# Performance work log

Measured on AMD Instinct MI355X. Metric: run time of the kernel, lower is better.

Reference implementation:

```python
import jax, jax.numpy as jnp
import numpy as np

N_SVC, N_NODE, N_POD = 50000, 20000, 100000
F = 128          # svc/instance/node feature dims (all 128 per init_kwargs)
HID = 128        # hidden_size
OUT = 64         # out_channel
E_SVC, E_PN, E_NP = 1600000, 100000, 100000


def _graph_conv(x, src, dst, n_src, n_dst, W, b):
    """DGL GraphConv with norm='both': D_dst^{-1/2} A D_src^{-1/2} X W + b."""
    ones = jnp.ones(src.shape[0], dtype=x.dtype)
    deg_src = jnp.clip(jax.ops.segment_sum(ones, src, num_segments=n_src), 1.0)
    deg_dst = jnp.clip(jax.ops.segment_sum(ones, dst, num_segments=n_dst), 1.0)
    # normalize at source, gather, scatter-sum to dst, normalize at dst
    h = x * jax.lax.rsqrt(deg_src)[:, None]          # [n_src, F]
    msg = h[src]                                      # [E, F] gather (memory-bound)
    agg = jax.ops.segment_sum(msg, dst, num_segments=n_dst)  # [n_dst, F]
    agg = agg * jax.lax.rsqrt(deg_dst)[:, None]
    return agg @ W + b                                # [n_dst, HID]


def _leaky(h):
    return jnp.where(h > 0, h, 0.01 * h)


def setup_inputs() -> dict:
    key = jax.random.key(0)
    ks = jax.random.split(key, 16)
    d = {
        "x_svc": jax.random.normal(ks[0], (N_SVC, F), jnp.float32),
        "x_pod": jax.random.normal(ks[1], (N_POD, F), jnp.float32),
        "x_node": jax.random.normal(ks[2], (N_NODE, F), jnp.float32),
        "svc_src": jax.random.randint(ks[3], (E_SVC,), 0, N_SVC, jnp.int32),
        "svc_dst": jax.random.randint(ks[4], (E_SVC,), 0, N_SVC, jnp.int32),
        "pod_node_src": jax.random.randint(ks[5], (E_PN,), 0, N_POD, jnp.int32),
        "pod_node_dst": jax.random.randint(ks[6], (E_PN,), 0, N_NODE, jnp.int32),
        "node_pod_src": jax.random.randint(ks[7], (E_NP,), 0, N_NODE, jnp.int32),
        "node_pod_dst": jax.random.randint(ks[8], (E_NP,), 0, N_POD, jnp.int32),
        # GraphConv weights per edge type
        "W_call": jax.random.normal(ks[9], (F, HID), jnp.float32) * (1.0 / np.sqrt(F)),
        "b_call": jnp.zeros((HID,), jnp.float32),
        "W_in": jax.random.normal(ks[10], (F, HID), jnp.float32) * (1.0 / np.sqrt(F)),
        "b_in": jnp.zeros((HID,), jnp.float32),
        "W_ni": jax.random.normal(ks[11], (F, HID), jnp.float32) * (1.0 / np.sqrt(F)),
        "b_ni": jnp.zeros((HID,), jnp.float32),
        # per-node-type output Linear (hidden -> out_channel)
        "W_lin_svc": jax.random.normal(ks[12], (HID, OUT), jnp.float32) * (1.0 / np.sqrt(HID)),
        "b_lin_svc": jnp.zeros((OUT,), jnp.float32),
        "W_lin_node": jax.random.normal(ks[13], (HID, OUT), jnp.float32) * (1.0 / np.sqrt(HID)),
        "b_lin_node": jnp.zeros((OUT,), jnp.float32),
        "W_lin_pod": jax.random.normal(ks[14], (HID, OUT), jnp.float32) * (1.0 / np.sqrt(HID)),
        "b_lin_pod": jnp.zeros((OUT,), jnp.float32),
    }
    return d


def reference(x_svc, x_pod, x_node,
              svc_src, svc_dst, pod_node_src, pod_node_dst,
              node_pod_src, node_pod_dst,
              W_call, b_call, W_in, b_in, W_ni, b_ni,
              W_lin_svc, b_lin_svc, W_lin_node, b_lin_node,
              W_lin_pod, b_lin_pod):
    # HeteroGraphConv (sum aggregate; each dst type receives one edge type here)
    h_svc = _graph_conv(x_svc, svc_src, svc_dst, N_SVC, N_SVC, W_call, b_call)
    h_node = _graph_conv(x_pod, pod_node_src, pod_node_dst, N_POD, N_NODE, W_in, b_in)
    h_pod = _graph_conv(x_node, node_pod_src, node_pod_dst, N_NODE, N_POD, W_ni, b_ni)
    # per-node-type LeakyReLU + Linear
    o_svc = _leaky(h_svc) @ W_lin_svc + b_lin_svc    # [N_SVC, OUT]
    o_node = _leaky(h_node) @ W_lin_node + b_lin_node  # [N_NODE, OUT]
    o_pod = _leaky(h_pod) @ W_lin_pod + b_lin_pod    # [N_POD, OUT]
    return jnp.concatenate([o_svc, o_node, o_pod], axis=0)  # [N_SVC+N_NODE+N_POD, OUT]
```

## Files before the change

kernel.cpp:

```cpp
#include <hip/hip_runtime.h>

typedef __attribute__((ext_vector_type(8))) short short8;
typedef __attribute__((ext_vector_type(4))) float floatx4;

#define N_SVC  50000
#define N_NODE 20000
#define N_POD  100000
#define E_SVC  1600000
#define E_PN   100000
#define E_NP   100000
#define N_TOT  170000
#define E_TOT  1800000
#define NBUCK  1329
#define NBLK   256
#define PER_BLK 7032
#define P_SVC_BASE  0
#define P_NODE_BASE 50048
#define P_POD_BASE  70080
#define P_TOT       170112
#define SVC_WAVES   50048
#define SVC_HALF    25024
#define SVC_HBLK    6256
#define NP_WAVES    30016
#define NP_BLOCKS   7504

__device__ __forceinline__ unsigned short f2bf(float f) {
  union { float f; unsigned u; } v; v.f = f;
  unsigned r = v.u + 0x7FFFu + ((v.u >> 16) & 1u);
  return (unsigned short)(r >> 16);
}
__device__ __forceinline__ unsigned pack_bf2(float a, float b) {
  return (unsigned)f2bf(a) | ((unsigned)f2bf(b) << 16);
}
__device__ __forceinline__ float bfl(unsigned u) { union { unsigned u; float f; } v; v.u = u << 16; return v.f; }
__device__ __forceinline__ float bfh(unsigned u) { union { unsigned u; float f; } v; v.u = u & 0xFFFF0000u; return v.f; }

__device__ __forceinline__ int dbase_of(int b) {
  if (b <= 391) return b * 6144;
  if (b <= 547) return 2402304 + (b - 391) * 1536;
  return 2641920 + (b - 547) * 512;
}
#define DST_CAP_TOT 3042304
__device__ __forceinline__ int sbase_of(int b) {
  if (b <= 391) return b * 6144;
  if (b <= 1171) return 2402304 + (b - 391) * 512;
  return 2801664 + (b - 1171) * 1536;
}
#define SRC_CAP_TOT 3044352

__device__ __forceinline__ void load_edge(int i,
    const int* __restrict__ svcS, const int* __restrict__ svcD,
    const int* __restrict__ pnS, const int* __restrict__ pnD,
    const int* __restrict__ npS, const int* __restrict__ npD,
    int& S, int& D) {
  if (i < E_SVC)             { S = svcS[i];                         D = svcD[i]; }
  else if (i < E_SVC + E_PN) { int j = i - E_SVC;        S = pnS[j] + 50000;  D = pnD[j] + 50000; }
  else                       { int j = i - E_SVC - E_PN; S = npS[j] + 150000; D = npD[j] + 70000; }
}

__global__ void wprep_init(const float* __restrict__ W0, const float* __restrict__ W1,
                           const float* __restrict__ W2, const float* __restrict__ L0,
                           const float* __restrict__ L1, const float* __restrict__ L2,
                           unsigned short* __restrict__ Wt, unsigned short* __restrict__ Wt2,
                           int* __restrict__ dcur, int* __restrict__ scur) {
  int i = blockIdx.x * 256 + threadIdx.x;
  if (i < NBUCK) { dcur[i] = dbase_of(i); scur[i] = sbase_of(i); }
  if (i < 3 * 16384) {
    int t = i / 16384, r = i % 16384, n = r / 128, k = r % 128;
    const float* W = (t == 0) ? W0 : ((t == 1) ? W1 : W2);
    Wt[i] = f2bf(W[k * 128 + n]);
  } else if (i < 3 * 16384 + 3 * 8192) {
    int j = i - 3 * 16384;
    int t = j / 8192, r = j % 8192, n = r / 128, k = r % 128;
    const float* L = (t == 0) ? L0 : ((t == 1) ? L1 : L2);
    Wt2[j] = f2bf(L[k * 64 + n]);
  }
}

__global__ __launch_bounds__(1024) void scatter_onepass(
    const int* __restrict__ svcS, const int* __restrict__ svcD,
    const int* __restrict__ pnS, const int* __restrict__ pnD,
    const int* __restrict__ npS, const int* __restrict__ npD,
    int* __restrict__ dcur, int* __restrict__ scur,
    unsigned* __restrict__ dstbuf, unsigned char* __restrict__ srcbuf) {
  __shared__ int ldc[NBUCK], lsc[NBUCK];
  const int tid = threadIdx.x;
  for (int t = tid; t < NBUCK; t += 1024) { ldc[t] = 0; lsc[t] = 0; }
  __syncthreads();
  const int lo = blockIdx.x * PER_BLK;
  const int hi = (lo + PER_BLK < E_TOT) ? lo + PER_BLK : E_TOT;
  int Sv[7], Dv[7];
  #pragma unroll
  for (int k = 0; k < 7; ++k) {
    int e = lo + tid + k * 1024;
    if (e < hi) {
      load_edge(e, svcS, svcD, pnS, pnD, npS, npD, Sv[k], Dv[k]);
      atomicAdd(&ldc[Dv[k] >> 7], 1);
      atomicAdd(&lsc[Sv[k] >> 7], 1);
    } else Sv[k] = -1;
  }
  __syncthreads();
  for (int t = tid; t < NBUCK; t += 1024) {
    int c = ldc[t];  ldc[t] = c ? atomicAdd(&dcur[t], c) : 0;
    int c2 = lsc[t]; lsc[t] = c2 ? atomicAdd(&scur[t], c2) : 0;
  }
  __syncthreads();
  #pragma unroll
  for (int k = 0; k < 7; ++k) {
    if (Sv[k] >= 0) {
      int p = atomicAdd(&ldc[Dv[k] >> 7], 1);
      dstbuf[p] = ((unsigned)(Dv[k] & 127) << 18) | (unsigned)Sv[k];
      int q = atomicAdd(&lsc[Sv[k] >> 7], 1);
      srcbuf[q] = (unsigned char)(Sv[k] & 127);
    }
  }
}

__global__ __launch_bounds__(256) void finalize_all(
    const int* __restrict__ dcur, const int* __restrict__ scur,
    const unsigned* __restrict__ dstbuf, const unsigned char* __restrict__ srcbuf,
    int2* __restrict__ rowrange, int* __restrict__ csr, int* __restrict__ cnt_src) {
  __shared__ int lcnt[128], lcur[128];
  __shared__ int s_w0;
  const int tid = threadIdx.x;
  if (blockIdx.x < NBUCK) {
    const int b = blockIdx.x;
    const int base = dbase_of(b);
    const int cnt = dcur[b] - base;
    if (tid < 128) lcnt[tid] = 0;
    __syncthreads();
    for (int e = tid; e < cnt; e += 256) atomicAdd(&lcnt[dstbuf[base + e] >> 18], 1);
    __syncthreads();
    int excl = 0, v = 0;
    if (tid < 128) {
      v = lcnt[tid];
      int lane = tid & 63;
      int x = v;
      #pragma unroll
      for (int off = 1; off < 64; off <<= 1) {
        int y = __shfl_up(x, off, 64);
        if (lane >= off) x += y;
      }
      excl = x - v;
      if (tid == 63) s_w0 = x;
    }
    __syncthreads();
    if (tid < 128) {
      if (tid >= 64) excl += s_w0;
      lcur[tid] = excl;
      int u = b * 128 + tid;
      if (u < N_TOT) rowrange[u] = make_int2(base + excl, base + excl + v);
    }
    __syncthreads();
    for (int e = tid; e < cnt; e += 256) {
      unsigned wv = dstbuf[base + e];
      int p = atomicAdd(&lcur[wv >> 18], 1);
      csr[base + p] = (int)(wv & 0x3FFFFu);
    }
  } else {
    const int b = blockIdx.x - NBUCK;
    const int base = sbase_of(b);
    const int cnt = scur[b] - base;
    if (tid < 128) lcnt[tid] = 0;
    __syncthreads();
    for (int e = tid; e < cnt; e += 256) atomicAdd(&lcnt[srcbuf[base + e]], 1);
    __syncthreads();
    if (tid < 128) {
      int u = b * 128 + tid;
      if (u < N_TOT) cnt_src[u] = lcnt[tid];
    }
  }
}

__global__ void normalize_cast(const float* __restrict__ xs, const int* __restrict__ cs,
                               unsigned* __restrict__ Xn) {
  int i = blockIdx.x * blockDim.x + threadIdx.x;
  if (i >= N_SVC * 32) return;
  int row = i >> 5, c4 = i & 31;
  const float* src = xs + (size_t)row * 128;
  int cc = cs[row]; if (cc < 1) cc = 1;
  float r = rsqrtf((float)cc);
  float4 v = ((const float4*)src)[c4];
  uint2 o;
  o.x = pack_bf2(v.x * r, v.y * r);
  o.y = pack_bf2(v.z * r, v.w * r);
  *(uint2*)(Xn + (size_t)row * 64 + c4 * 2) = o;
}

#define ACC8(v) { a0 += bfl(v.x); a1 += bfh(v.x); a2 += bfl(v.y); a3 += bfh(v.y); \
                  a4 += bfl(v.z); a5 += bfh(v.z); a6 += bfl(v.w); a7 += bfh(v.w); }

__global__ __launch_bounds__(256) void aggregate_svc(
    const unsigned* __restrict__ Xn, const int2* __restrict__ rowrange,
    const int* __restrict__ csr, unsigned* __restrict__ aggb, int rbase) {
  const int lane = threadIdx.x & 63;
  const int gw = rbase + blockIdx.x * 4 + (threadIdx.x >> 6);
  const int grp = lane >> 4, l16 = lane & 15;
  const unsigned* Xb = Xn + l16 * 4;
  unsigned* orow = aggb + (size_t)gw * 64 + l16 * 4;
  if (gw >= 50000) {
    if (gw < SVC_WAVES && grp == 0) *(uint4*)orow = (uint4){0u, 0u, 0u, 0u};
    return;
  }
  int2 rr = rowrange[gw];
  int beg = rr.x, end = rr.y;
  int deg = end - beg;
  float a0 = 0.f, a1 = 0.f, a2 = 0.f, a3 = 0.f, a4 = 0.f, a5 = 0.f, a6 = 0.f, a7 = 0.f;
  int e = beg;
  for (; e + 16 <= end; e += 16) {
    int s0 = csr[e + grp];
    int s1 = csr[e + 4 + grp];
    int s2 = csr[e + 8 + grp];
    int s3 = csr[e + 12 + grp];
    uint4 v0 = *(const uint4*)(Xb + (unsigned)s0 * 64);
    uint4 v1 = *(const uint4*)(Xb + (unsigned)s1 * 64);
    uint4 v2 = *(const uint4*)(Xb + (unsigned)s2 * 64);
    uint4 v3 = *(const uint4*)(Xb + (unsigned)s3 * 64);
    ACC8(v0) ACC8(v1) ACC8(v2) ACC8(v3)
  }
  for (; e + 8 <= end; e += 8) {
    int s0 = csr[e + grp];
    int s1 = csr[e + 4 + grp];
    uint4 v0 = *(const uint4*)(Xb + (unsigned)s0 * 64);
    uint4 v1 = *(const uint4*)(Xb + (unsigned)s1 * 64);
    ACC8(v0) ACC8(v1)
  }
  for (; e + 4 <= end; e += 4) {
    int s = csr[e + grp];
    uint4 v = *(const uint4*)(Xb + (unsigned)s * 64);
    ACC8(v)
  }
  if (grp < end - e) {
    int s = csr[e + grp];
    uint4 v = *(const uint4*)(Xb + (unsigned)s * 64);
    ACC8(v)
  }
  a0 += __shfl_xor(a0, 32, 64); a1 += __shfl_xor(a1, 32, 64);
  a2 += __shfl_xor(a2, 32, 64); a3 += __shfl_xor(a3, 32, 64);
  a4 += __shfl_xor(a4, 32, 64); a5 += __shfl_xor(a5, 32, 64);
  a6 += __shfl_xor(a6, 32, 64); a7 += __shfl_xor(a7, 32, 64);
  a0 += __shfl_xor(a0, 16, 64); a1 += __shfl_xor(a1, 16, 64);
  a2 += __shfl_xor(a2, 16, 64); a3 += __shfl_xor(a3, 16, 64);
  a4 += __shfl_xor(a4, 16, 64); a5 += __shfl_xor(a5, 16, 64);
  a6 += __shfl_xor(a6, 16, 64); a7 += __shfl_xor(a7, 16, 64);
  float rd = rsqrtf((float)(deg < 1 ? 1 : deg));
  if (grp == 0) {
    uint4 o;
    o.x = pack_bf2(a0 * rd, a1 * rd);
    o.y = pack_bf2(a2 * rd, a3 * rd);
    o.z = pack_bf2(a4 * rd, a5 * rd);
    o.w = pack_bf2(a6 * rd, a7 * rd);
    *(uint4*)orow = o;
  }
}

__global__ __launch_bounds__(256) void aggregate_np(
    const float* __restrict__ xp, const float* __restrict__ xn,
    const int* __restrict__ cnt_src, const int2* __restrict__ rowrange,
    const int* __restrict__ csr, unsigned* __restrict__ aggb) {
  const int lane = threadIdx.x & 63;
  const int w = blockIdx.x * 4 + (threadIdx.x >> 6);
  const int grp = lane >> 4, l16 = lane & 15;
  const int row = SVC_WAVES + w * 4 + grp;
  if (row >= P_TOT) return;
  int u; bool valid; const float* Xf; int soff;
  if (row < P_POD_BASE) { u = row - 48; valid = (row - P_NODE_BASE) < 20000; Xf = xp; soff = 50000; }
  else                  { u = row - 80; valid = (row - P_POD_BASE) < 100000; Xf = xn; soff = 150000; }
  unsigned* orow = aggb + (size_t)row * 64 + l16 * 4;
  if (!valid) {
    *(uint4*)orow = (uint4){0u, 0u, 0u, 0u};
    return;
  }
  const float* Xb = Xf + l16 * 8;
  int2 rr = rowrange[u];
  int beg = rr.x, end = rr.y;
  int deg = end - beg;
  float a0 = 0.f, a1 = 0.f, a2 = 0.f, a3 = 0.f, a4 = 0.f, a5 = 0.f, a6 = 0.f, a7 = 0.f;
  int e = beg;
  for (; e + 2 <= end; e += 2) {
    int s0 = csr[e], s1 = csr[e + 1];
    int c0 = cnt_src[s0]; if (c0 < 1) c0 = 1;
    int c1 = cnt_src[s1]; if (c1 < 1) c1 = 1;
    float r0 = rsqrtf((float)c0), r1 = rsqrtf((float)c1);
    const float* p0 = Xb + (size_t)(s0 - soff) * 128;
    const float* p1 = Xb + (size_t)(s1 - soff) * 128;
    float4 u0 = *(const float4*)p0;
    float4 u1 = *(const float4*)(p0 + 4);
    float4 w0 = *(const float4*)p1;
    float4 w1 = *(const float4*)(p1 + 4);
    a0 += u0.x * r0 + w0.x * r1; a1 += u0.y * r0 + w0.y * r1;
    a2 += u0.z * r0 + w0.z * r1; a3 += u0.w * r0 + w0.w * r1;
    a4 += u1.x * r0 + w1.x * r1; a5 += u1.y * r0 + w1.y * r1;
    a6 += u1.z * r0 + w1.z * r1; a7 += u1.w * r0 + w1.w * r1;
  }
  if (e < end) {
    int s = csr[e];
    int c = cnt_src[s]; if (c < 1) c = 1;
    float r = rsqrtf((float)c);
    const float* p = Xb + (size_t)(s - soff) * 128;
    float4 u0 = *(const float4*)p;
    float4 u1 = *(const float4*)(p + 4);
    a0 += u0.x * r; a1 += u0.y * r; a2 += u0.z * r; a3 += u0.w * r;
    a4 += u1.x * r; a5 += u1.y * r; a6 += u1.z * r; a7 += u1.w * r;
  }
  float rd = rsqrtf((float)(deg < 1 ? 1 : deg));
  uint4 o;
  o.x = pack_bf2(a0 * rd, a1 * rd);
  o.y = pack_bf2(a2 * rd, a3 * rd);
  o.z = pack_bf2(a4 * rd, a5 * rd);
  o.w = pack_bf2(a6 * rd, a7 * rd);
  *(uint4*)orow = o;
}

__global__ __launch_bounds__(256) void gemm_fused(
    const unsigned short* __restrict__ aggb,
    const unsigned short* __restrict__ Wt,
    const unsigned short* __restrict__ Wt2,
    const float* __restrict__ b0, const float* __restrict__ b1, const float* __restrict__ b2,
    const float* __restrict__ l0, const float* __restrict__ l1, const float* __restrict__ l2,
    float* __restrict__ out) {
  __shared__ __align__(16) unsigned short sW1[128 * 136];
  __shared__ __align__(16) unsigned short sH[4][16 * 136];
  const int bid = blockIdx.x;
  int t, bl, nb, ntile, padbase, outbase, mcnt;
  if (bid < 226)      { t = 0; bl = bid;       nb = 226; ntile = 782;  padbase = P_SVC_BASE;  outbase = 0;     mcnt = 50000; }
  else if (bid < 316) { t = 1; bl = bid - 226; nb = 90;  ntile = 313;  padbase = P_NODE_BASE; outbase = 50000; mcnt = 20000; }
  else                { t = 2; bl = bid - 316; nb = 452; ntile = 1563; padbase = P_POD_BASE;  outbase = 70000; mcnt = 100000; }
  const float* bp = (t == 0) ? b0 : ((t == 1) ? b1 : b2);
  const float* lp = (t == 0) ? l0 : ((t == 1) ? l1 : l2);

  const unsigned short* W1g = Wt + t * 16384;
  for (int uu = threadIdx.x; uu < 2048; uu += 256) {
    short8 v = *(const short8*)(W1g + uu * 8);
    *(short8*)(&sW1[(uu >> 4) * 136 + (uu & 15) * 8]) = v;
  }
  const int wv = threadIdx.x >> 6, lane = threadIdx.x & 63;
  const int quad = lane >> 4, l16 = lane & 15;

  const unsigned short* W2g = Wt2 + t * 8192;
  short8 w2f[4][4];
  #pragma unroll
  for (int n = 0; n < 4; n++)
    #pragma unroll
    for (int kt = 0; kt < 4; kt++)
      w2f[n][kt] = *(const short8*)(W2g + (n * 16 + l16) * 128 + kt * 32 + quad * 8);
  float bias1[8], bias2[4];
  #pragma unroll
  for (int n = 0; n < 8; n++) bias1[n] = bp[n * 16 + l16];
  #pragma unroll
  for (int n = 0; n < 4; n++) bias2[n] = lp[n * 16 + l16];
  __syncthreads();

  const unsigned short* Abase = aggb + (size_t)padbase * 128
                              + (size_t)(wv * 16 + l16) * 128 + quad * 8;
  short8 afc[4];
  if (bl < ntile) {
    const unsigned short* Ar = Abase + (size_t)bl * 8192;
    #pragma unroll
    for (int kt = 0; kt < 4; kt++) afc[kt] = *(const short8*)(Ar + kt * 32);
  }
  for (int tile = bl; tile < ntile; tile += nb) {
    short8 afn[4] = {afc[0], afc[1], afc[2], afc[3]};
    int tn = tile + nb;
    if (tn < ntile) {
      const unsigned short* Ar = Abase + (size_t)tn * 8192;
      #pragma unroll
      for (int kt = 0; kt < 4; kt++) afn[kt] = *(const short8*)(Ar + kt * 32);
    }
    floatx4 acc[8];
    #pragma unroll
    for (int n = 0; n < 8; n++) acc[n] = (floatx4){0.f, 0.f, 0.f, 0.f};
    #pragma unroll
    for (int kt = 0; kt < 4; kt++) {
      #pragma unroll
      for (int n = 0; n < 8; n++) {
        short8 bf = *(const short8*)(&sW1[(n * 16 + l16) * 136 + kt * 32 + quad * 8]);
        acc[n] = __builtin_amdgcn_mfma_f32_16x16x32_bf16(afc[kt], bf, acc[n], 0, 0, 0);
      }
    }
    #pragma unroll
    for (int n = 0; n < 8; n++) {
      #pragma unroll
      for (int i = 0; i < 4; i++) {
        float h = acc[n][i] + bias1[n];
        h = (h > 0.f) ? h : 0.01f * h;
        sH[wv][(quad * 4 + i) * 136 + n * 16 + l16] = f2bf(h);
      }
    }
    floatx4 acc2[4];
    #pragma unroll
    for (int n = 0; n < 4; n++) acc2[n] = (floatx4){0.f, 0.f, 0.f, 0.f};
    #pragma unroll
    for (int kt = 0; kt < 4; kt++) {
      short8 af = *(const short8*)(&sH[wv][l16 * 136 + kt * 32 + quad * 8]);
      #pragma unroll
      for (int n = 0; n < 4; n++)
        acc2[n] = __builtin_amdgcn_mfma_f32_16x16x32_bf16(af, w2f[n][kt], acc2[n], 0, 0, 0);
    }
    int r0 = tile * 64 + wv * 16 + quad * 4;
    #pragma unroll
    for (int n = 0; n < 4; n++) {
      #pragma unroll
      for (int i = 0; i < 4; i++) {
        int r = r0 + i;
        if (r < mcnt) out[(size_t)(outbase + r) * 64 + n * 16 + l16] = acc2[n][i] + bias2[n];
      }
    }
    #pragma unroll
    for (int kt = 0; kt < 4; kt++) afc[kt] = afn[kt];
  }
}

extern "C" void kernel_launch(void* const* d_in, const int* in_sizes, int n_in,
                              void* d_out, int out_size, void* d_ws, size_t ws_size,
                              hipStream_t stream) {
  const float* x_svc  = (const float*)d_in[0];
  const float* x_pod  = (const float*)d_in[1];
  const float* x_node = (const float*)d_in[2];
  const int* svc_src  = (const int*)d_in[3];
  const int* svc_dst  = (const int*)d_in[4];
  const int* pn_src   = (const int*)d_in[5];
  const int* pn_dst   = (const int*)d_in[6];
  const int* np_src   = (const int*)d_in[7];
  const int* np_dst   = (const int*)d_in[8];
  const float* W_call = (const float*)d_in[9];
  const float* b_call = (const float*)d_in[10];
  const float* W_in   = (const float*)d_in[11];
  const float* b_in   = (const float*)d_in[12];
  const float* W_ni   = (const float*)d_in[13];
  const float* b_ni   = (const float*)d_in[14];
  const float* W_ls   = (const float*)d_in[15];
  const float* b_ls   = (const float*)d_in[16];
  const float* W_ln   = (const float*)d_in[17];
  const float* b_ln   = (const float*)d_in[18];
  const float* W_lp   = (const float*)d_in[19];
  const float* b_lp   = (const float*)d_in[20];
  float* out = (float*)d_out;

  char* ws = (char*)d_ws;
  int*  dcur     = (int*)(ws + 0);
  int*  scur     = (int*)(ws + 5504);
  int2* rowrange = (int2*)(ws + 11008);
  int*  cnt_src  = (int*)(ws + 1371008);
  int*  csr      = (int*)(ws + 2051072);
  unsigned short* Wt  = (unsigned short*)(ws + 14220288);
  unsigned short* Wt2 = (unsigned short*)(ws + 14318592);
  unsigned* Xn     = (unsigned*)(ws + 14367744);
  unsigned* dstbuf = (unsigned*)(ws + 14367744);
  unsigned char* srcbuf = (unsigned char*)(ws + 27180032);
  unsigned* aggb   = (unsigned*)(ws + 30224384);

  wprep_init<<<288, 256, 0, stream>>>(W_call, W_in, W_ni, W_ls, W_ln, W_lp,
                                      Wt, Wt2, dcur, scur);
  scatter_onepass<<<NBLK, 1024, 0, stream>>>(svc_src, svc_dst, pn_src, pn_dst,
                                             np_src, np_dst, dcur, scur, dstbuf, srcbuf);
  finalize_all<<<2 * NBUCK, 256, 0, stream>>>(dcur, scur, dstbuf, srcbuf,
                                              rowrange, csr, cnt_src);
  normalize_cast<<<6250, 256, 0, stream>>>(x_svc, cnt_src, Xn);
  aggregate_svc<<<SVC_HBLK, 256, 0, stream>>>(Xn, rowrange, csr, aggb, 0);
  aggregate_svc<<<SVC_HBLK, 256, 0, stream>>>(Xn, rowrange, csr, aggb, SVC_HALF);
  aggregate_np<<<NP_BLOCKS, 256, 0, stream>>>(x_pod, x_node, cnt_src, rowrange, csr, aggb);
  gemm_fused<<<768, 256, 0, stream>>>((const unsigned short*)aggb, Wt, Wt2,
                                      b_call, b_in, b_ni, b_ls, b_ln, b_lp, out);
}
```

Measured before the change: 307.0 us.

## Fuse normalize-cast into finalize and merge aggregation kernels into one launch

Folds the source-degree normalization and bf16 cast of svc features into the source-count blocks of finalize_all. Xn moves to its own workspace region so it no longer aliases dstbuf. The two svc aggregation launches and the pod/node aggregation launch become a single aggregate_all kernel that branches on wave index. The A-fragment register prefetch in gemm_fused is also removed. The goal is fewer kernel launches and inter-kernel gaps, at the cost of less-coalesced per-thread row writes in the cast and losing the GEMM prefetch.

```diff
diff --git a/kernel.cpp b/kernel.cpp
--- a/kernel.cpp
+++ b/kernel.cpp
@@ -19,10 +19,8 @@
 #define P_POD_BASE  70080
 #define P_TOT       170112
 #define SVC_WAVES   50048
-#define SVC_HALF    25024
-#define SVC_HBLK    6256
-#define NP_WAVES    30016
-#define NP_BLOCKS   7504
+#define AGG_WAVES   80064
+#define AGG_BLOCKS  20016
 
 __device__ __forceinline__ unsigned short f2bf(float f) {
   union { float f; unsigned u; } v; v.f = f;
@@ -119,7 +117,8 @@
 __global__ __launch_bounds__(256) void finalize_all(
     const int* __restrict__ dcur, const int* __restrict__ scur,
     const unsigned* __restrict__ dstbuf, const unsigned char* __restrict__ srcbuf,
-    int2* __restrict__ rowrange, int* __restrict__ csr, int* __restrict__ cnt_src) {
+    int2* __restrict__ rowrange, int* __restrict__ csr, int* __restrict__ cnt_src,
+    const float* __restrict__ xs, unsigned* __restrict__ Xn) {
   __shared__ int lcnt[128], lcur[128];
   __shared__ int s_w0;
   const int tid = threadIdx.x;
@@ -169,82 +168,138 @@
       int u = b * 128 + tid;
       if (u < N_TOT) cnt_src[u] = lcnt[tid];
     }
-  }
-}
-
-__global__ void normalize_cast(const float* __restrict__ xs, const int* __restrict__ cs,
-                               unsigned* __restrict__ Xn) {
-  int i = blockIdx.x * blockDim.x + threadIdx.x;
-  if (i >= N_SVC * 32) return;
-  int row = i >> 5, c4 = i & 31;
-  const float* src = xs + (size_t)row * 128;
-  int cc = cs[row]; if (cc < 1) cc = 1;
-  float r = rsqrtf((float)cc);
-  float4 v = ((const float4*)src)[c4];
-  uint2 o;
-  o.x = pack_bf2(v.x * r, v.y * r);
-  o.y = pack_bf2(v.z * r, v.w * r);
-  *(uint2*)(Xn + (size_t)row * 64 + c4 * 2) = o;
+    if (b <= 391) {
+      int row = b * 128 + (tid >> 1);
+      int half = tid & 1;
+      if (row < N_SVC) {
+        int cc = lcnt[tid >> 1]; if (cc < 1) cc = 1;
+        float r = rsqrtf((float)cc);
+        const float* src = xs + (size_t)row * 128 + half * 64;
+        unsigned* dst = Xn + (size_t)row * 64 + half * 32;
+        #pragma unroll
+        for (int q = 0; q < 16; q++) {
+          float4 v = ((const float4*)src)[q];
+          dst[2 * q]     = pack_bf2(v.x * r, v.y * r);
+          dst[2 * q + 1] = pack_bf2(v.z * r, v.w * r);
+        }
+      }
+    }
+  }
 }
 
 #define ACC8(v) { a0 += bfl(v.x); a1 += bfh(v.x); a2 += bfl(v.y); a3 += bfh(v.y); \
                   a4 += bfl(v.z); a5 += bfh(v.z); a6 += bfl(v.w); a7 += bfh(v.w); }
 
-__global__ __launch_bounds__(256) void aggregate_svc(
+__global__ __launch_bounds__(256) void aggregate_all(
     const unsigned* __restrict__ Xn, const int2* __restrict__ rowrange,
-    const int* __restrict__ csr, unsigned* __restrict__ aggb, int rbase) {
+    const int* __restrict__ csr, const float* __restrict__ xp,
+    const float* __restrict__ xnode, const int* __restrict__ cnt_src,
+    unsigned* __restrict__ aggb) {
   const int lane = threadIdx.x & 63;
-  const int gw = rbase + blockIdx.x * 4 + (threadIdx.x >> 6);
+  const int gwave = blockIdx.x * 4 + (threadIdx.x >> 6);
   const int grp = lane >> 4, l16 = lane & 15;
-  const unsigned* Xb = Xn + l16 * 4;
-  unsigned* orow = aggb + (size_t)gw * 64 + l16 * 4;
-  if (gw >= 50000) {
-    if (gw < SVC_WAVES && grp == 0) *(uint4*)orow = (uint4){0u, 0u, 0u, 0u};
-    return;
-  }
-  int2 rr = rowrange[gw];
-  int beg = rr.x, end = rr.y;
-  int deg = end - beg;
-  float a0 = 0.f, a1 = 0.f, a2 = 0.f, a3 = 0.f, a4 = 0.f, a5 = 0.f, a6 = 0.f, a7 = 0.f;
-  int e = beg;
-  for (; e + 16 <= end; e += 16) {
-    int s0 = csr[e + grp];
-    int s1 = csr[e + 4 + grp];
-    int s2 = csr[e + 8 + grp];
-    int s3 = csr[e + 12 + grp];
-    uint4 v0 = *(const uint4*)(Xb + (unsigned)s0 * 64);
-    uint4 v1 = *(const uint4*)(Xb + (unsigned)s1 * 64);
-    uint4 v2 = *(const uint4*)(Xb + (unsigned)s2 * 64);
-    uint4 v3 = *(const uint4*)(Xb + (unsigned)s3 * 64);
-    ACC8(v0) ACC8(v1) ACC8(v2) ACC8(v3)
-  }
-  for (; e + 8 <= end; e += 8) {
-    int s0 = csr[e + grp];
-    int s1 = csr[e + 4 + grp];
-    uint4 v0 = *(const uint4*)(Xb + (unsigned)s0 * 64);
-    uint4 v1 = *(const uint4*)(Xb + (unsigned)s1 * 64);
-    ACC8(v0) ACC8(v1)
-  }
-  for (; e + 4 <= end; e += 4) {
-    int s = csr[e + grp];
-    uint4 v = *(const uint4*)(Xb + (unsigned)s * 64);
-    ACC8(v)
-  }
-  if (grp < end - e) {
-    int s = csr[e + grp];
-    uint4 v = *(const uint4*)(Xb + (unsigned)s * 64);
-    ACC8(v)
-  }
-  a0 += __shfl_xor(a0, 32, 64); a1 += __shfl_xor(a1, 32, 64);
-  a2 += __shfl_xor(a2, 32, 64); a3 += __shfl_xor(a3, 32, 64);
-  a4 += __shfl_xor(a4, 32, 64); a5 += __shfl_xor(a5, 32, 64);
-  a6 += __shfl_xor(a6, 32, 64); a7 += __shfl_xor(a7, 32, 64);
-  a0 += __shfl_xor(a0, 16, 64); a1 += __shfl_xor(a1, 16, 64);
-  a2 += __shfl_xor(a2, 16, 64); a3 += __shfl_xor(a3, 16, 64);
-  a4 += __shfl_xor(a4, 16, 64); a5 += __shfl_xor(a5, 16, 64);
-  a6 += __shfl_xor(a6, 16, 64); a7 += __shfl_xor(a7, 16, 64);
-  float rd = rsqrtf((float)(deg < 1 ? 1 : deg));
-  if (grp == 0) {
+  if (gwave < SVC_WAVES) {
+    const int gw = gwave;
+    const unsigned* Xb = Xn + l16 * 4;
+    unsigned* orow = aggb + (size_t)gw * 64 + l16 * 4;
+    if (gw >= 50000) {
+      if (grp == 0) *(uint4*)orow = (uint4){0u, 0u, 0u, 0u};
+      return;
+    }
+    int2 rr = rowrange[gw];
+    int beg = rr.x, end = rr.y;
+    int deg = end - beg;
+    float a0 = 0.f, a1 = 0.f, a2 = 0.f, a3 = 0.f, a4 = 0.f, a5 = 0.f, a6 = 0.f, a7 = 0.f;
+    int e = beg;
+    for (; e + 16 <= end; e += 16) {
+      int s0 = csr[e + grp];
+      int s1 = csr[e + 4 + grp];
+      int s2 = csr[e + 8 + grp];
+      int s3 = csr[e + 12 + grp];
+      uint4 v0 = *(const uint4*)(Xb + (unsigned)s0 * 64);
+      uint4 v1 = *(const uint4*)(Xb + (unsigned)s1 * 64);
+      uint4 v2 = *(const uint4*)(Xb + (unsigned)s2 * 64);
+      uint4 v3 = *(const uint4*)(Xb + (unsigned)s3 * 64);
+      ACC8(v0) ACC8(v1) ACC8(v2) ACC8(v3)
+    }
+    for (; e + 8 <= end; e += 8) {
+      int s0 = csr[e + grp];
+      int s1 = csr[e + 4 + grp];
+      uint4 v0 = *(const uint4*)(Xb + (unsigned)s0 * 64);
+      uint4 v1 = *(const uint4*)(Xb + (unsigned)s1 * 64);
+      ACC8(v0) ACC8(v1)
+    }
+    for (; e + 4 <= end; e += 4) {
+      int s = csr[e + grp];
+      uint4 v = *(const uint4*)(Xb + (unsigned)s * 64);
+      ACC8(v)
+    }
+    if (grp < end - e) {
+      int s = csr[e + grp];
+      uint4 v = *(const uint4*)(Xb + (unsigned)s * 64);
+      ACC8(v)
+    }
+    a0 += __shfl_xor(a0, 32, 64); a1 += __shfl_xor(a1, 32, 64);
+    a2 += __shfl_xor(a2, 32, 64); a3 += __shfl_xor(a3, 32, 64);
+    a4 += __shfl_xor(a4, 32, 64); a5 += __shfl_xor(a5, 32, 64);
+    a6 += __shfl_xor(a6, 32, 64); a7 += __shfl_xor(a7, 32, 64);
+    a0 += __shfl_xor(a0, 16, 64); a1 += __shfl_xor(a1, 16, 64);
+    a2 += __shfl_xor(a2, 16, 64); a3 += __shfl_xor(a3, 16, 64);
+    a4 += __shfl_xor(a4, 16, 64); a5 += __shfl_xor(a5, 16, 64);
+    a6 += __shfl_xor(a6, 16, 64); a7 += __shfl_xor(a7, 16, 64);
+    float rd = rsqrtf((float)(deg < 1 ? 1 : deg));
+    if (grp == 0) {
+      uint4 o;
+      o.x = pack_bf2(a0 * rd, a1 * rd);
+      o.y = pack_bf2(a2 * rd, a3 * rd);
+      o.z = pack_bf2(a4 * rd, a5 * rd);
+      o.w = pack_bf2(a6 * rd, a7 * rd);
+      *(uint4*)orow = o;
+    }
+  } else {
+    const int row = SVC_WAVES + (gwave - SVC_WAVES) * 4 + grp;
+    if (row >= P_TOT) return;
+    int u; bool valid; const float* Xf; int soff;
+    if (row < P_POD_BASE) { u = row - 48; valid = (row - P_NODE_BASE) < 20000; Xf = xp;    soff = 50000; }
+    else                  { u = row - 80; valid = (row - P_POD_BASE) < 100000; Xf = xnode; soff = 150000; }
+    unsigned* orow = aggb + (size_t)row * 64 + l16 * 4;
+    if (!valid) {
+      *(uint4*)orow = (uint4){0u, 0u, 0u, 0u};
+      return;
+    }
+    const float* Xb = Xf + l16 * 8;
+    int2 rr = rowrange[u];
+    int beg = rr.x, end = rr.y;
+    int deg = end - beg;
+    float a0 = 0.f, a1 = 0.f, a2 = 0.f, a3 = 0.f, a4 = 0.f, a5 = 0.f, a6 = 0.f, a7 = 0.f;
+    int e = beg;
+    for (; e + 2 <= end; e += 2) {
+      int s0 = csr[e], s1 = csr[e + 1];
+      int c0 = cnt_src[s0]; if (c0 < 1) c0 = 1;
+      int c1 = cnt_src[s1]; if (c1 < 1) c1 = 1;
+      float r0 = rsqrtf((float)c0), r1 = rsqrtf((float)c1);
+      const float* p0 = Xb + (size_t)(s0 - soff) * 128;
+      const float* p1 = Xb + (size_t)(s1 - soff) * 128;
+      float4 u0 = *(const float4*)p0;
+      float4 u1 = *(const float4*)(p0 + 4);
+      float4 w0 = *(const float4*)p1;
+      float4 w1 = *(const float4*)(p1 + 4);
+      a0 += u0.x * r0 + w0.x * r1; a1 += u0.y * r0 + w0.y * r1;
+      a2 += u0.z * r0 + w0.z * r1; a3 += u0.w * r0 + w0.w * r1;
+      a4 += u1.x * r0 + w1.x * r1; a5 += u1.y * r0 + w1.y * r1;
+      a6 += u1.z * r0 + w1.z * r1; a7 += u1.w * r0 + w1.w * r1;
+    }
+    if (e < end) {
+      int s = csr[e];
+      int c = cnt_src[s]; if (c < 1) c = 1;
+      float r = rsqrtf((float)c);
+      const float* p = Xb + (size_t)(s - soff) * 128;
+      float4 u0 = *(const float4*)p;
+      float4 u1 = *(const float4*)(p + 4);
+      a0 += u0.x * r; a1 += u0.y * r; a2 += u0.z * r; a3 += u0.w * r;
+      a4 += u1.x * r; a5 += u1.y * r; a6 += u1.z * r; a7 += u1.w * r;
+    }
+    float rd = rsqrtf((float)(deg < 1 ? 1 : deg));
     uint4 o;
     o.x = pack_bf2(a0 * rd, a1 * rd);
     o.y = pack_bf2(a2 * rd, a3 * rd);
@@ -252,64 +307,6 @@
     o.w = pack_bf2(a6 * rd, a7 * rd);
     *(uint4*)orow = o;
   }
-}
-
-__global__ __launch_bounds__(256) void aggregate_np(
-    const float* __restrict__ xp, const float* __restrict__ xn,
-    const int* __restrict__ cnt_src, const int2* __restrict__ rowrange,
-    const int* __restrict__ csr, unsigned* __restrict__ aggb) {
-  const int lane = threadIdx.x & 63;
-  const int w = blockIdx.x * 4 + (threadIdx.x >> 6);
-  const int grp = lane >> 4, l16 = lane & 15;
-  const int row = SVC_WAVES + w * 4 + grp;
-  if (row >= P_TOT) return;
-  int u; bool valid; const float* Xf; int soff;
-  if (row < P_POD_BASE) { u = row - 48; valid = (row - P_NODE_BASE) < 20000; Xf = xp; soff = 50000; }
-  else                  { u = row - 80; valid = (row - P_POD_BASE) < 100000; Xf = xn; soff = 150000; }
-  unsigned* orow = aggb + (size_t)row * 64 + l16 * 4;
-  if (!valid) {
-    *(uint4*)orow = (uint4){0u, 0u, 0u, 0u};
-    return;
-  }
-  const float* Xb = Xf + l16 * 8;
-  int2 rr = rowrange[u];
-  int beg = rr.x, end = rr.y;
-  int deg = end - beg;
-  float a0 = 0.f, a1 = 0.f, a2 = 0.f, a3 = 0.f, a4 = 0.f, a5 = 0.f, a6 = 0.f, a7 = 0.f;
-  int e = beg;
-  for (; e + 2 <= end; e += 2) {
-    int s0 = csr[e], s1 = csr[e + 1];
-    int c0 = cnt_src[s0]; if (c0 < 1) c0 = 1;
-    int c1 = cnt_src[s1]; if (c1 < 1) c1 = 1;
-    float r0 = rsqrtf((float)c0), r1 = rsqrtf((float)c1);
-    const float* p0 = Xb + (size_t)(s0 - soff) * 128;
-    const float* p1 = Xb + (size_t)(s1 - soff) * 128;
-    float4 u0 = *(const float4*)p0;
-    float4 u1 = *(const float4*)(p0 + 4);
-    float4 w0 = *(const float4*)p1;
-    float4 w1 = *(const float4*)(p1 + 4);
-    a0 += u0.x * r0 + w0.x * r1; a1 += u0.y * r0 + w0.y * r1;
-    a2 += u0.z * r0 + w0.z * r1; a3 += u0.w * r0 + w0.w * r1;
-    a4 += u1.x * r0 + w1.x * r1; a5 += u1.y * r0 + w1.y * r1;
-    a6 += u1.z * r0 + w1.z * r1; a7 += u1.w * r0 + w1.w * r1;
-  }
-  if (e < end) {
-    int s = csr[e];
-    int c = cnt_src[s]; if (c < 1) c = 1;
-    float r = rsqrtf((float)c);
-    const float* p = Xb + (size_t)(s - soff) * 128;
-    float4 u0 = *(const float4*)p;
-    float4 u1 = *(const float4*)(p + 4);
-    a0 += u0.x * r; a1 += u0.y * r; a2 += u0.z * r; a3 += u0.w * r;
-    a4 += u1.x * r; a5 += u1.y * r; a6 += u1.z * r; a7 += u1.w * r;
-  }
-  float rd = rsqrtf((float)(deg < 1 ? 1 : deg));
-  uint4 o;
-  o.x = pack_bf2(a0 * rd, a1 * rd);
-  o.y = pack_bf2(a2 * rd, a3 * rd);
-  o.z = pack_bf2(a4 * rd, a5 * rd);
-  o.w = pack_bf2(a6 * rd, a7 * rd);
-  *(uint4*)orow = o;
 }
 
 __global__ __launch_bounds__(256) void gemm_fused(
@@ -351,31 +348,18 @@
   for (int n = 0; n < 4; n++) bias2[n] = lp[n * 16 + l16];
   __syncthreads();
 
-  const unsigned short* Abase = aggb + (size_t)padbase * 128
-                              + (size_t)(wv * 16 + l16) * 128 + quad * 8;
-  short8 afc[4];
-  if (bl < ntile) {
-    const unsigned short* Ar = Abase + (size_t)bl * 8192;
-    #pragma unroll
-    for (int kt = 0; kt < 4; kt++) afc[kt] = *(const short8*)(Ar + kt * 32);
-  }
   for (int tile = bl; tile < ntile; tile += nb) {
-    short8 afn[4] = {afc[0], afc[1], afc[2], afc[3]};
-    int tn = tile + nb;
-    if (tn < ntile) {
-      const unsigned short* Ar = Abase + (size_t)tn * 8192;
-      #pragma unroll
-      for (int kt = 0; kt < 4; kt++) afn[kt] = *(const short8*)(Ar + kt * 32);
-    }
+    const unsigned short* Arow = aggb + (size_t)(padbase + tile * 64 + wv * 16 + l16) * 128;
     floatx4 acc[8];
     #pragma unroll
     for (int n = 0; n < 8; n++) acc[n] = (floatx4){0.f, 0.f, 0.f, 0.f};
     #pragma unroll
     for (int kt = 0; kt < 4; kt++) {
+      short8 af = *(const short8*)(Arow + kt * 32 + quad * 8);
       #pragma unroll
       for (int n = 0; n < 8; n++) {
         short8 bf = *(const short8*)(&sW1[(n * 16 + l16) * 136 + kt * 32 + quad * 8]);
-        acc[n] = __builtin_amdgcn_mfma_f32_16x16x32_bf16(afc[kt], bf, acc[n], 0, 0, 0);
+        acc[n] = __builtin_amdgcn_mfma_f32_16x16x32_bf16(af, bf, acc[n], 0, 0, 0);
       }
     }
     #pragma unroll
@@ -406,8 +390,6 @@
         if (r < mcnt) out[(size_t)(outbase + r) * 64 + n * 16 + l16] = acc2[n][i] + bias2[n];
       }
     }
-    #pragma unroll
-    for (int kt = 0; kt < 4; kt++) afc[kt] = afn[kt];
   }
 }
 
@@ -445,21 +427,19 @@
   int*  csr      = (int*)(ws + 2051072);
   unsigned short* Wt  = (unsigned short*)(ws + 14220288);
   unsigned short* Wt2 = (unsigned short*)(ws + 14318592);
-  unsigned* Xn     = (unsigned*)(ws + 14367744);
   unsigned* dstbuf = (unsigned*)(ws + 14367744);
   unsigned char* srcbuf = (unsigned char*)(ws + 27180032);
   unsigned* aggb   = (unsigned*)(ws + 30224384);
+  unsigned* Xn     = (unsigned*)(ws + 73773056);
 
   wprep_init<<<288, 256, 0, stream>>>(W_call, W_in, W_ni, W_ls, W_ln, W_lp,
                                       Wt, Wt2, dcur, scur);
   scatter_onepass<<<NBLK, 1024, 0, stream>>>(svc_src, svc_dst, pn_src, pn_dst,
                                              np_src, np_dst, dcur, scur, dstbuf, srcbuf);
   finalize_all<<<2 * NBUCK, 256, 0, stream>>>(dcur, scur, dstbuf, srcbuf,
-                                              rowrange, csr, cnt_src);
-  normalize_cast<<<6250, 256, 0, stream>>>(x_svc, cnt_src, Xn);
-  aggregate_svc<<<SVC_HBLK, 256, 0, stream>>>(Xn, rowrange, csr, aggb, 0);
-  aggregate_svc<<<SVC_HBLK, 256, 0, stream>>>(Xn, rowrange, csr, aggb, SVC_HALF);
-  aggregate_np<<<NP_BLOCKS, 256, 0, stream>>>(x_pod, x_node, cnt_src, rowrange, csr, aggb);
+                                              rowrange, csr, cnt_src, x_svc, Xn);
+  aggregate_all<<<AGG_BLOCKS, 256, 0, stream>>>(Xn, rowrange, csr, x_pod, x_node,
+                                                cnt_src, aggb);
   gemm_fused<<<768, 256, 0, stream>>>((const unsigned short*)aggb, Wt, Wt2,
                                       b_call, b_in, b_ni, b_ls, b_ln, b_lp, out);
 }
```

New measurement: 307.6 us. About the same (+0.2%).
